# Optimization experiments

Measured on AMD Instinct MI355X. Metric: run time of the kernel, lower is better.

## Reference

```python
import jax, jax.numpy as jnp
import numpy as np

NUM_STEPS = 5  # matches init num_steps
N_NODES = 500_000
N_EDGES = 32_000_000


def setup_inputs() -> dict:
    key = jax.random.key(0)
    k1, k2, k3 = jax.random.split(key, 3)
    prior_probs = jax.random.uniform(k1, (N_NODES,), dtype=jnp.float32)
    edge_index = jax.random.randint(k2, (2, N_EDGES), 0, N_NODES, dtype=jnp.int32)
    edge_probs = jax.random.uniform(k3, (N_EDGES,), dtype=jnp.float32)
    return {"prior_probs": prior_probs, "edge_index": edge_index, "edge_probs": edge_probs}


def reference(prior_probs, edge_index, edge_probs):
    num_nodes = prior_probs.shape[0]
    source = edge_index[0]
    target = edge_index[1]
    p_t_u = prior_probs
    prod_terms = jnp.ones_like(prior_probs)
    for _ in range(NUM_STEPS):
        # gather node activation at source, weight by edge prob, scatter-add into target
        message = edge_probs * p_t_u[source]            # [E]
        agg = jax.ops.segment_sum(message, target, num_segments=num_nodes)  # [N]
        delta = 1.0 - jnp.exp(-agg)
        new_p_t_u = prod_terms * delta
        prod_terms = prod_terms * (1.0 - new_p_t_u)
        p_t_u = new_p_t_u
    p_final = 1.0 - prod_terms + prior_probs
    return p_final.reshape(-1, 1)
```

## Files before the change

### kernel.cpp

```cpp
#include <hip/hip_runtime.h>

#define NUM_STEPS 5
typedef unsigned int u32;

#define RSH 10
#define RSZ 1024
#define SB  256
#define ST  512
#define SRC_BITS 19
#define SRC_MASK 0x7FFFFu

static inline size_t align256(size_t x){ return (x + 255) & ~(size_t)255; }


__global__ void init_fast(const float* __restrict__ prior, float* __restrict__ p0,
                          float* __restrict__ prod, int n){
    int i = blockIdx.x*blockDim.x + threadIdx.x;
    if(i<n){ p0[i]=prior[i]; prod[i]=1.0f; }
}

__global__ void hist_kernel(const int* __restrict__ dst, long long E, int B,
                            u32* __restrict__ blk_cnt){
    extern __shared__ u32 hist[];
    int sb = blockIdx.x;
    long long E4 = E >> 2;
    long long chunk = (E4 + SB - 1)/SB;
    long long i0 = (long long)sb*chunk;
    long long i1 = i0 + chunk; if(i1 > E4) i1 = E4;
    for(int b=threadIdx.x; b<B; b+=blockDim.x) hist[b]=0;
    __syncthreads();
    const int4* d4 = (const int4*)dst;
    for(long long i=i0+threadIdx.x; i<i1; i+=blockDim.x){
        int4 d = d4[i];
        atomicAdd(&hist[((u32)d.x)>>RSH], 1u);
        atomicAdd(&hist[((u32)d.y)>>RSH], 1u);
        atomicAdd(&hist[((u32)d.z)>>RSH], 1u);
        atomicAdd(&hist[((u32)d.w)>>RSH], 1u);
    }
    if(sb==0){
        for(long long e=(E4<<2)+threadIdx.x; e<E; e+=blockDim.x)
            atomicAdd(&hist[((u32)dst[e])>>RSH], 1u);
    }
    __syncthreads();
    for(int b=threadIdx.x; b<B; b+=blockDim.x) blk_cnt[(size_t)sb*B + b] = hist[b];
}

__global__ void colscan_kernel(u32* __restrict__ blk_cnt, int B, u32* __restrict__ tot){
    __shared__ u32 s[SB];
    int b = blockIdx.x, t = threadIdx.x;
    u32 v = blk_cnt[(size_t)t*B + b];
    s[t] = v; __syncthreads();
    for(int off=1; off<SB; off<<=1){
        u32 x = (t>=off) ? s[t-off] : 0;
        __syncthreads();
        s[t] += x;
        __syncthreads();
    }
    blk_cnt[(size_t)t*B + b] = s[t] - v;
    if(t==SB-1) tot[b] = s[SB-1];
}

__global__ void basescan_kernel(const u32* __restrict__ tot, u32* __restrict__ base, int B){
    __shared__ u32 s[256];
    int t = threadIdx.x;
    u32 v0 = (2*t   < B) ? tot[2*t]   : 0;
    u32 v1 = (2*t+1 < B) ? tot[2*t+1] : 0;
    u32 sum = v0 + v1;
    s[t] = sum; __syncthreads();
    for(int off=1; off<256; off<<=1){
        u32 x = (t>=off) ? s[t-off] : 0;
        __syncthreads();
        s[t] += x;
        __syncthreads();
    }
    u32 run = s[t] - sum;
    if(2*t   < B) base[2*t]   = run;
    if(2*t+1 < B) base[2*t+1] = run + v0;
    if(t==255) base[B] = s[255];
}

__global__ void scatter_kernel(const int* __restrict__ src, const int* __restrict__ dst,
                               const float* __restrict__ ep, long long E, int B,
                               const u32* __restrict__ blk_rel, const u32* __restrict__ base,
                               uint2* __restrict__ edges){
    extern __shared__ u32 cur[];
    int sb = blockIdx.x;
    long long E4 = E >> 2;
    long long chunk = (E4 + SB - 1)/SB;
    long long i0 = (long long)sb*chunk;
    long long i1 = i0 + chunk; if(i1 > E4) i1 = E4;
    for(int b=threadIdx.x; b<B; b+=blockDim.x)
        cur[b] = base[b] + blk_rel[(size_t)sb*B + b];
    __syncthreads();
    const int4*   s4 = (const int4*)src;
    const int4*   d4 = (const int4*)dst;
    const float4* w4 = (const float4*)ep;
    for(long long i=i0+threadIdx.x; i<i1; i+=blockDim.x){
        int4 s = s4[i]; int4 d = d4[i]; float4 w = w4[i];
        u32 dd, pos;
        dd=(u32)d.x; pos=atomicAdd(&cur[dd>>RSH],1u);
        edges[pos]=make_uint2(((u32)s.x)|((dd&(RSZ-1))<<SRC_BITS), __float_as_uint(w.x));
        dd=(u32)d.y; pos=atomicAdd(&cur[dd>>RSH],1u);
        edges[pos]=make_uint2(((u32)s.y)|((dd&(RSZ-1))<<SRC_BITS), __float_as_uint(w.y));
        dd=(u32)d.z; pos=atomicAdd(&cur[dd>>RSH],1u);
        edges[pos]=make_uint2(((u32)s.z)|((dd&(RSZ-1))<<SRC_BITS), __float_as_uint(w.z));
        dd=(u32)d.w; pos=atomicAdd(&cur[dd>>RSH],1u);
        edges[pos]=make_uint2(((u32)s.w)|((dd&(RSZ-1))<<SRC_BITS), __float_as_uint(w.w));
    }
    if(sb==0){
        for(long long e=(E4<<2)+threadIdx.x; e<E; e+=blockDim.x){
            u32 dd=(u32)dst[e];
            u32 pos=atomicAdd(&cur[dd>>RSH],1u);
            edges[pos]=make_uint2(((u32)src[e])|((dd&(RSZ-1))<<SRC_BITS), __float_as_uint(ep[e]));
        }
    }
}

__global__ __launch_bounds__(512) void
step_kernel(const uint2* __restrict__ edges, const u32* __restrict__ base,
            const float* __restrict__ p_cur, float* __restrict__ p_nxt,
            float* __restrict__ prod, const float* __restrict__ prior,
            float* __restrict__ out, int n, int final_step){
    __shared__ float acc[2][RSZ];
    int b = blockIdx.x, t = threadIdx.x;
    for(int k=t; k<RSZ; k+=blockDim.x){ acc[0][k]=0.0f; acc[1][k]=0.0f; }
    __syncthreads();
    u32 e0 = base[b], e1 = base[b+1];
    int rep = t & 1;
    for(u32 e = e0 + t; e < e1; e += blockDim.x){
        uint2 pk = edges[e];
        float m = __uint_as_float(pk.y) * p_cur[pk.x & SRC_MASK];
        atomicAdd(&acc[rep][pk.x >> SRC_BITS], m);
    }
    __syncthreads();
    int i0 = b << RSH;
    for(int k=t; k<RSZ; k+=blockDim.x){
        int i = i0 + k;
        if(i < n){
            float a = acc[0][k] + acc[1][k];
            float pr_old = prod[i];
            float np = pr_old * (1.0f - expf(-a));
            float pr = pr_old * (1.0f - np);
            prod[i]  = pr;
            p_nxt[i] = np;
            if(final_step) out[i] = 1.0f - pr + prior[i];
        }
    }
}


__global__ void init_kernel(const float* __restrict__ prior, float* __restrict__ p,
                            float* __restrict__ prod, float* __restrict__ agg, int n){
    int i = blockIdx.x*blockDim.x + threadIdx.x;
    if(i<n){ p[i]=prior[i]; prod[i]=1.0f; agg[i]=0.0f; }
}

__global__ void edge_kernel(const int* __restrict__ src, const int* __restrict__ dst,
                            const float* __restrict__ ep, const float* __restrict__ p,
                            float* __restrict__ agg, int e4, int e_rem, long long e4base){
    int i = blockIdx.x*blockDim.x + threadIdx.x;
    if(i < e4){
        int4   s = ((const int4*)src)[i];
        int4   t = ((const int4*)dst)[i];
        float4 w = ((const float4*)ep)[i];
        atomicAdd(&agg[t.x], w.x * p[s.x]);
        atomicAdd(&agg[t.y], w.y * p[s.y]);
        atomicAdd(&agg[t.z], w.z * p[s.z]);
        atomicAdd(&agg[t.w], w.w * p[s.w]);
    }
    if(blockIdx.x==0 && threadIdx.x < e_rem){
        long long e = e4base + threadIdx.x;
        atomicAdd(&agg[dst[e]], ep[e]*p[src[e]]);
    }
}

__global__ void node_kernel(float* __restrict__ p, float* __restrict__ prod,
                            float* __restrict__ agg, const float* __restrict__ prior,
                            float* __restrict__ out, int n, int final_step){
    int i = blockIdx.x*blockDim.x + threadIdx.x;
    if(i<n){
        float a = agg[i]; agg[i]=0.0f;
        float pr_old = prod[i];
        float np = pr_old*(1.0f - expf(-a));
        float pr = pr_old*(1.0f - np);
        prod[i]=pr; p[i]=np;
        if(final_step) out[i] = 1.0f - pr + prior[i];
    }
}


extern "C" void kernel_launch(void* const* d_in, const int* in_sizes, int n_in,
                              void* d_out, int out_size, void* d_ws, size_t ws_size,
                              hipStream_t stream){
    const float* prior = (const float*)d_in[0];
    const int*   eidx  = (const int*)d_in[1];
    const float* ep    = (const float*)d_in[2];

    const int n = in_sizes[0];
    const long long E = (long long)in_sizes[2];
    const int* src = eidx;
    const int* dst = eidx + E;
    float* out = (float*)d_out;

    const int B = (n + RSZ - 1) >> RSH;

    size_t szN   = align256((size_t)n * 4);
    size_t szB1  = align256((size_t)(B + 1) * 4);
    size_t szB   = align256((size_t)B * 4);
    size_t szCnt = align256((size_t)SB * B * 4);
    size_t szE2  = align256((size_t)E * 8);

    size_t off_p0   = 0;
    size_t off_p1   = off_p0 + szN;
    size_t off_prod = off_p1 + szN;
    size_t off_base = off_prod + szN;
    size_t off_tot  = off_base + szB1;
    size_t off_cnt  = off_tot + szB;
    size_t off_edge = off_cnt + szCnt;
    size_t need     = off_edge + szE2;

    char* ws = (char*)d_ws;

    if(ws_size >= need && n < (1 << SRC_BITS) && B <= 512){
        float* p0    = (float*)(ws + off_p0);
        float* p1    = (float*)(ws + off_p1);
        float* prod  = (float*)(ws + off_prod);
        u32*   base  = (u32*)  (ws + off_base);
        u32*   tot   = (u32*)  (ws + off_tot);
        u32*   cnt   = (u32*)  (ws + off_cnt);
        uint2* edges = (uint2*)(ws + off_edge);

        const int nb_n = (n + 255)/256;
        init_fast<<<nb_n, 256, 0, stream>>>(prior, p0, prod, n);
        hist_kernel<<<SB, ST, (size_t)B*4, stream>>>(dst, E, B, cnt);
        colscan_kernel<<<B, SB, 0, stream>>>(cnt, B, tot);
        basescan_kernel<<<1, 256, 0, stream>>>(tot, base, B);
        scatter_kernel<<<SB, ST, (size_t)B*4, stream>>>(src, dst, ep, E, B, cnt, base, edges);

        float* pc = p0;
        float* pn = p1;
        for(int step=0; step<NUM_STEPS; ++step){
            step_kernel<<<B, 512, 0, stream>>>(edges, base, pc, pn, prod, prior, out,
                                               n, step == NUM_STEPS-1 ? 1 : 0);
            float* t2 = pc; pc = pn; pn = t2;
        }
    } else {
        float* p    = (float*)d_ws;
        float* prod = p + n;
        float* agg  = prod + n;
        const int nb_n = (n + 255)/256;
        init_kernel<<<nb_n, 256, 0, stream>>>(prior, p, prod, agg, n);
        const int e4 = (int)(E/4);
        const int e_rem = (int)(E%4);
        const long long e4base = (long long)e4*4;
        const int nb_e = (e4 + 255)/256;
        for(int step=0; step<NUM_STEPS; ++step){
            edge_kernel<<<nb_e, 256, 0, stream>>>(src, dst, ep, p, agg, e4, e_rem, e4base);
            node_kernel<<<nb_n, 256, 0, stream>>>(p, prod, agg, prior, out, n,
                                                  step == NUM_STEPS-1 ? 1 : 0);
        }
    }
}
```

Measured before the change: 1.339 ms.

## Split each destination bucket across two blocks, store node probabilities as half

Each destination bucket's edge range is now split between two blocks. Each block writes its partial sums to a global buffer, and a separate combine kernel adds the two partials and applies the node update. This doubles the grid (about 489 blocks up to about 978), which should fill the GPU's CUs better. Node probabilities are stored as fp16 to halve the gather footprint, and the histogram and scatter use twice as many superblocks. In exchange it adds an extra kernel launch per step, a global round trip for the partials, and reduced precision in the propagated probabilities, which may break the accuracy tolerance.

```diff
diff --git a/kernel.cpp b/kernel.cpp
--- a/kernel.cpp
+++ b/kernel.cpp
@@ -1,22 +1,24 @@
 #include <hip/hip_runtime.h>
+#include <hip/hip_fp16.h>
 
 #define NUM_STEPS 5
 typedef unsigned int u32;
 
 #define RSH 10
 #define RSZ 1024
-#define SB  256
+#define SB  512
 #define ST  512
+#define SPLIT 2
 #define SRC_BITS 19
 #define SRC_MASK 0x7FFFFu
 
 static inline size_t align256(size_t x){ return (x + 255) & ~(size_t)255; }
 
 
-__global__ void init_fast(const float* __restrict__ prior, float* __restrict__ p0,
+__global__ void init_fast(const float* __restrict__ prior, __half* __restrict__ p,
                           float* __restrict__ prod, int n){
     int i = blockIdx.x*blockDim.x + threadIdx.x;
-    if(i<n){ p0[i]=prior[i]; prod[i]=1.0f; }
+    if(i<n){ p[i]=__float2half_rn(prior[i]); prod[i]=1.0f; }
 }
 
 __global__ void hist_kernel(const int* __restrict__ dst, long long E, int B,
@@ -118,33 +120,43 @@
 
 __global__ __launch_bounds__(512) void
 step_kernel(const uint2* __restrict__ edges, const u32* __restrict__ base,
-            const float* __restrict__ p_cur, float* __restrict__ p_nxt,
-            float* __restrict__ prod, const float* __restrict__ prior,
-            float* __restrict__ out, int n, int final_step){
+            const __half* __restrict__ p, float* __restrict__ pacc){
     __shared__ float acc[2][RSZ];
-    int b = blockIdx.x, t = threadIdx.x;
+    int blk = blockIdx.x;
+    int b   = blk >> 1;
+    int part= blk & 1;
+    int t   = threadIdx.x;
     for(int k=t; k<RSZ; k+=blockDim.x){ acc[0][k]=0.0f; acc[1][k]=0.0f; }
     __syncthreads();
     u32 e0 = base[b], e1 = base[b+1];
+    u32 cnt = e1 - e0;
+    u32 s0 = e0 + (cnt*part)/SPLIT;
+    u32 s1 = e0 + (cnt*(part+1))/SPLIT;
     int rep = t & 1;
-    for(u32 e = e0 + t; e < e1; e += blockDim.x){
+    for(u32 e = s0 + t; e < s1; e += blockDim.x){
         uint2 pk = edges[e];
-        float m = __uint_as_float(pk.y) * p_cur[pk.x & SRC_MASK];
-        atomicAdd(&acc[rep][pk.x >> SRC_BITS], m);
-    }
-    __syncthreads();
-    int i0 = b << RSH;
-    for(int k=t; k<RSZ; k+=blockDim.x){
-        int i = i0 + k;
-        if(i < n){
-            float a = acc[0][k] + acc[1][k];
-            float pr_old = prod[i];
-            float np = pr_old * (1.0f - expf(-a));
-            float pr = pr_old * (1.0f - np);
-            prod[i]  = pr;
-            p_nxt[i] = np;
-            if(final_step) out[i] = 1.0f - pr + prior[i];
-        }
+        float pv = __half2float(p[pk.x & SRC_MASK]);
+        atomicAdd(&acc[rep][pk.x >> SRC_BITS], __uint_as_float(pk.y) * pv);
+    }
+    __syncthreads();
+    float* dstp = pacc + (size_t)blk * RSZ;
+    for(int k=t; k<RSZ; k+=blockDim.x) dstp[k] = acc[0][k] + acc[1][k];
+}
+
+__global__ void combine_kernel(const float* __restrict__ pacc, __half* __restrict__ p,
+                               float* __restrict__ prod, const float* __restrict__ prior,
+                               float* __restrict__ out, int n, int final_step){
+    int i = blockIdx.x*blockDim.x + threadIdx.x;
+    if(i < n){
+        int b = i >> RSH, k = i & (RSZ-1);
+        float a = pacc[(size_t)(b*SPLIT    )*RSZ + k]
+                + pacc[(size_t)(b*SPLIT + 1)*RSZ + k];
+        float pr_old = prod[i];
+        float np = pr_old * (1.0f - expf(-a));
+        float pr = pr_old * (1.0f - np);
+        prod[i] = pr;
+        p[i] = __float2half_rn(np);
+        if(final_step) out[i] = 1.0f - pr + prior[i];
     }
 }
 
@@ -204,45 +216,45 @@
 
     const int B = (n + RSZ - 1) >> RSH;
 
+    size_t szNh  = align256((size_t)n * 2);
     size_t szN   = align256((size_t)n * 4);
     size_t szB1  = align256((size_t)(B + 1) * 4);
     size_t szB   = align256((size_t)B * 4);
     size_t szCnt = align256((size_t)SB * B * 4);
+    size_t szAcc = align256((size_t)SPLIT * B * RSZ * 4);
     size_t szE2  = align256((size_t)E * 8);
 
-    size_t off_p0   = 0;
-    size_t off_p1   = off_p0 + szN;
-    size_t off_prod = off_p1 + szN;
+    size_t off_p    = 0;
+    size_t off_prod = off_p + szNh;
     size_t off_base = off_prod + szN;
     size_t off_tot  = off_base + szB1;
     size_t off_cnt  = off_tot + szB;
-    size_t off_edge = off_cnt + szCnt;
+    size_t off_acc  = off_cnt + szCnt;
+    size_t off_edge = off_acc + szAcc;
     size_t need     = off_edge + szE2;
 
     char* ws = (char*)d_ws;
 
     if(ws_size >= need && n < (1 << SRC_BITS) && B <= 512){
-        float* p0    = (float*)(ws + off_p0);
-        float* p1    = (float*)(ws + off_p1);
-        float* prod  = (float*)(ws + off_prod);
-        u32*   base  = (u32*)  (ws + off_base);
-        u32*   tot   = (u32*)  (ws + off_tot);
-        u32*   cnt   = (u32*)  (ws + off_cnt);
-        uint2* edges = (uint2*)(ws + off_edge);
+        __half* p    = (__half*)(ws + off_p);
+        float*  prod = (float*) (ws + off_prod);
+        u32*    base = (u32*)   (ws + off_base);
+        u32*    tot  = (u32*)   (ws + off_tot);
+        u32*    cnt  = (u32*)   (ws + off_cnt);
+        float*  pacc = (float*) (ws + off_acc);
+        uint2*  edges= (uint2*) (ws + off_edge);
 
         const int nb_n = (n + 255)/256;
-        init_fast<<<nb_n, 256, 0, stream>>>(prior, p0, prod, n);
+        init_fast<<<nb_n, 256, 0, stream>>>(prior, p, prod, n);
         hist_kernel<<<SB, ST, (size_t)B*4, stream>>>(dst, E, B, cnt);
         colscan_kernel<<<B, SB, 0, stream>>>(cnt, B, tot);
         basescan_kernel<<<1, 256, 0, stream>>>(tot, base, B);
         scatter_kernel<<<SB, ST, (size_t)B*4, stream>>>(src, dst, ep, E, B, cnt, base, edges);
 
-        float* pc = p0;
-        float* pn = p1;
         for(int step=0; step<NUM_STEPS; ++step){
-            step_kernel<<<B, 512, 0, stream>>>(edges, base, pc, pn, prod, prior, out,
-                                               n, step == NUM_STEPS-1 ? 1 : 0);
-            float* t2 = pc; pc = pn; pn = t2;
+            step_kernel<<<B*SPLIT, 512, 0, stream>>>(edges, base, p, pacc);
+            combine_kernel<<<nb_n, 256, 0, stream>>>(pacc, p, prod, prior, out, n,
+                                                     step == NUM_STEPS-1 ? 1 : 0);
         }
     } else {
         float* p    = (float*)d_ws;
```

New measurement: 1.346 ms. Within noise of the previous version (+0.5%).
